# Kernel tuning notes

Hardware: AMD Instinct MI355X
Metric: run time of the kernel (lower is better)

The kernel has to match this reference:

```python
import jax, jax.numpy as jnp
import numpy as np

N_USERS = 100000
N_ITEMS = 50000
N_NODES = N_USERS + N_ITEMS
N_EDGES = 4800000
EMB = 64
N_LAYERS = 3
BATCH = 16384


def setup_inputs() -> dict:
    key = jax.random.key(0)
    ks = jax.random.split(key, 12)
    users = jax.random.randint(ks[0], (BATCH,), 0, N_USERS)
    pos_items = jax.random.randint(ks[1], (BATCH,), 0, N_ITEMS)
    neg_items = jax.random.randint(ks[2], (BATCH,), 0, N_ITEMS)
    rows = jax.random.randint(ks[3], (N_EDGES,), 0, N_NODES)
    cols = jax.random.randint(ks[4], (N_EDGES,), 0, N_NODES)
    vals = jax.random.uniform(ks[5], (N_EDGES,), dtype=jnp.float32)
    # learned parameters (xavier-ish scale)
    user_emb = jax.random.normal(ks[6], (N_USERS, EMB), dtype=jnp.float32) * 0.1
    item_emb = jax.random.normal(ks[7], (N_ITEMS, EMB), dtype=jnp.float32) * 0.1
    # Linear weights stored as [in, out] so y = x @ W + b (matches torch Linear math)
    W1s = jax.random.normal(ks[8], (N_LAYERS, EMB, EMB), dtype=jnp.float32) * (1.0 / np.sqrt(EMB))
    b1s = jnp.zeros((N_LAYERS, EMB), dtype=jnp.float32)
    W2s = jax.random.normal(ks[9], (N_LAYERS, EMB, EMB), dtype=jnp.float32) * (1.0 / np.sqrt(EMB))
    b2s = jnp.zeros((N_LAYERS, EMB), dtype=jnp.float32)
    return dict(users=users, pos_items=pos_items, neg_items=neg_items,
                rows=rows, cols=cols, vals=vals,
                user_emb=user_emb, item_emb=item_emb,
                W1s=W1s, b1s=b1s, W2s=W2s, b2s=b2s)


def _leaky_relu(x):
    return jnp.where(x > 0, x, 0.2 * x)


def _computer(user_emb, item_emb, rows, cols, vals, W1s, b1s, W2s, b2s):
    all_emb = jnp.concatenate([user_emb, item_emb], axis=0)  # [N, 64]
    embs = [all_emb]
    for i in range(N_LAYERS):
        self_emb = all_emb @ W1s[i] + b1s[i]
        # sparse adjacency SpMM: gather neighbor features, weight, segment-sum by row
        neighbor = jax.ops.segment_sum(vals[:, None] * all_emb[cols], rows,
                                       num_segments=N_NODES)
        neighbor = neighbor @ W2s[i] + b2s[i]
        interact = (neighbor * all_emb) @ W2s[i] + b2s[i]
        all_emb = _leaky_relu(self_emb + neighbor + interact)
        embs.append(all_emb)
    embs = jnp.concatenate(embs, axis=1)  # [N, 64*(n_layers+1)] = [N, 256]
    return embs[:N_USERS], embs[N_USERS:]


def reference(users, pos_items, neg_items, rows, cols, vals,
              user_emb, item_emb, W1s, b1s, W2s, b2s):
    all_users, all_items = _computer(user_emb, item_emb, rows, cols, vals,
                                     W1s, b1s, W2s, b2s)
    users_emb = all_users[users]
    pos_emb = all_items[pos_items]
    neg_emb = all_items[neg_items]
    return users_emb, pos_emb, neg_emb
```

## Files before the change

### kernel.cpp

```cpp
#include <hip/hip_runtime.h>


#define EMB 64

constexpr int kNUsers = 100000;
constexpr int kNItems = 50000;
constexpr int kNNodes = 150000;
constexpr int kNEdges = 4800000;
constexpr int kBatch  = 16384;
constexpr int kLayers = 3;
constexpr int kRngShift = 8;
constexpr int kNRanges  = (kNNodes + 255) >> 8;
constexpr int kEdgesPerBin = 16384;
constexpr int kBinBlocks = (kNEdges + kEdgesPerBin - 1) / kEdgesPerBin;
constexpr int kEPW    = 16;

__device__ __forceinline__ float f4c(const float4& v, int i) {
  return ((const float*)&v)[i];
}
__device__ __forceinline__ float4 f4fma(float s, float4 w, float4 a) {
  a.x = fmaf(s, w.x, a.x);
  a.y = fmaf(s, w.y, a.y);
  a.z = fmaf(s, w.z, a.z);
  a.w = fmaf(s, w.w, a.w);
  return a;
}
__device__ __forceinline__ float4 f4add(float4 a, float4 b) {
  a.x += b.x; a.y += b.y; a.z += b.z; a.w += b.w;
  return a;
}
__device__ __forceinline__ float lrelu(float x) { return x > 0.f ? x : 0.2f * x; }

#define F16(M) M(0) M(1) M(2) M(3) M(4) M(5) M(6) M(7) \
               M(8) M(9) M(10) M(11) M(12) M(13) M(14) M(15)

__global__ __launch_bounds__(256) void init_embed(
    const float* __restrict__ user_emb, const float* __restrict__ item_emb,
    float* __restrict__ cur)
{
  const size_t userF = (size_t)kNUsers * EMB;
  const size_t allF4 = (size_t)kNNodes * EMB / 4;
  const size_t i = (size_t)blockIdx.x * 256 + threadIdx.x;
  if (i >= allF4) return;
  const size_t f = i * 4;
  const float4 v = (f < userF) ? ((const float4*)user_emb)[i]
                               : ((const float4*)(item_emb))[(f - userF) / 4];
  ((float4*)cur)[i] = v;
}

__global__ __launch_bounds__(256) void quant8(
    const float* __restrict__ cur, signed char* __restrict__ cur8,
    float* __restrict__ rowScale)
{
  const int lane = threadIdx.x & 63;
  const int r = (blockIdx.x << 2) | (threadIdx.x >> 6);
  if (r >= kNNodes) return;
  const float v = cur[(size_t)r * EMB + lane];
  float m = fabsf(v);
#pragma unroll
  for (int off = 32; off >= 1; off >>= 1)
    m = fmaxf(m, __shfl_xor(m, off, 64));
  const float inv = (m > 0.f) ? (127.0f / m) : 0.f;
  cur8[(size_t)r * EMB + lane] = (signed char)__float2int_rn(v * inv);
  if (lane == 0) rowScale[r] = m * (1.0f / 127.0f);
}


__global__ __launch_bounds__(1024) void hist_ranges(
    const int* __restrict__ rows, int* __restrict__ rangeA)
{
  __shared__ int cnt[kNRanges];
  const int tid = threadIdx.x;
  const int e0  = blockIdx.x * kEdgesPerBin;
  int e1 = e0 + kEdgesPerBin;
  if (e1 > kNEdges) e1 = kNEdges;
  for (int b = tid; b < kNRanges; b += 1024) cnt[b] = 0;
  __syncthreads();
  for (int e = e0 + tid; e < e1; e += 1024)
    atomicAdd(&cnt[rows[e] >> kRngShift], 1);
  __syncthreads();
  for (int b = tid; b < kNRanges; b += 1024)
    if (cnt[b] > 0) atomicAdd(&rangeA[b], cnt[b]);
}

__global__ __launch_bounds__(1024) void scan_ranges(
    int* __restrict__ rangeA, int* __restrict__ rowPtr)
{
  __shared__ int wsum[16];
  const int tid  = threadIdx.x;
  const int lane = tid & 63;
  const int wid  = tid >> 6;
  const int cnt  = (tid < kNRanges) ? rangeA[tid] : 0;
  int v = cnt;
#pragma unroll
  for (int off = 1; off < 64; off <<= 1) {
    const int n = __shfl_up(v, off, 64);
    if (lane >= off) v += n;
  }
  if (lane == 63) wsum[wid] = v;
  __syncthreads();
  if (tid == 0) {
    int s = 0;
#pragma unroll
    for (int w = 0; w < 16; ++w) { const int t = wsum[w]; wsum[w] = s; s += t; }
  }
  __syncthreads();
  if (tid < kNRanges) rangeA[tid] = wsum[wid] + v - cnt;
  if (tid == 0) {
    rangeA[kNRanges]  = kNEdges;
    rowPtr[kNNodes]   = kNEdges;
  }
}

__global__ __launch_bounds__(1024) void bin_edges(
    const int* __restrict__ rows, const int* __restrict__ cols,
    const float* __restrict__ vals, const int* __restrict__ rangeA,
    int* __restrict__ rangeCnt, int2* __restrict__ tmpE)
{
  __shared__ int cnt[kNRanges];
  __shared__ int base[kNRanges];
  const int tid = threadIdx.x;
  const int e0  = blockIdx.x * kEdgesPerBin;
  int e1 = e0 + kEdgesPerBin;
  if (e1 > kNEdges) e1 = kNEdges;

  for (int b = tid; b < kNRanges; b += 1024) cnt[b] = 0;
  __syncthreads();
  for (int e = e0 + tid; e < e1; e += 1024)
    atomicAdd(&cnt[rows[e] >> kRngShift], 1);
  __syncthreads();
  for (int b = tid; b < kNRanges; b += 1024) {
    const int c = cnt[b];
    base[b] = (c > 0) ? (rangeA[b] + atomicAdd(&rangeCnt[b], c)) : 0;
    cnt[b] = 0;
  }
  __syncthreads();
  for (int e = e0 + tid; e < e1; e += 1024) {
    const int r = rows[e];
    const int b = r >> kRngShift;
    const int rank = atomicAdd(&cnt[b], 1);
    tmpE[base[b] + rank] =
        make_int2(cols[e] | ((r & 255) << 18), __float_as_int(vals[e]));
  }
}

__global__ __launch_bounds__(256) void place_edges(
    const int2* __restrict__ tmpE, const int* __restrict__ rangeA,
    int2* __restrict__ edgeS, int* __restrict__ rowPtr)
{
  __shared__ int lcnt[256];
  __shared__ int lbase[256];
  __shared__ int ws[4];
  const int b    = blockIdx.x;
  const int r0   = b << kRngShift;
  const int tid  = threadIdx.x;
  const int lane = tid & 63;
  const int wid  = tid >> 6;
  const int start = rangeA[b];
  const int end   = rangeA[b + 1];

  lcnt[tid] = 0;
  __syncthreads();
  for (int e = start + tid; e < end; e += 256)
    atomicAdd(&lcnt[(tmpE[e].x >> 18) & 255], 1);
  __syncthreads();

  const int c = lcnt[tid];
  int v = c;
#pragma unroll
  for (int off = 1; off < 64; off <<= 1) {
    const int n = __shfl_up(v, off, 64);
    if (lane >= off) v += n;
  }
  if (lane == 63) ws[wid] = v;
  __syncthreads();
  int wadd = 0;
#pragma unroll
  for (int w = 0; w < 4; ++w) if (w < wid) wadd += ws[w];
  const int excl = v - c + wadd;
  lbase[tid] = start + excl;
  if (r0 + tid < kNNodes) rowPtr[r0 + tid] = start + excl;
  lcnt[tid] = 0;
  __syncthreads();

  for (int e = start + tid; e < end; e += 256) {
    const int2 cv = tmpE[e];
    const int rl  = (cv.x >> 18) & 255;
    const int rank = atomicAdd(&lcnt[rl], 1);
    edgeS[lbase[rl] + rank] = make_int2(cv.x & 0x3FFFF, cv.y);
  }
}

__global__ __launch_bounds__(256) void spmm_csr8(
    const signed char* __restrict__ cur8, const float* __restrict__ rowScale,
    const int* __restrict__ rowPtr, const int2* __restrict__ edgeS,
    float* __restrict__ nbuf)
{
  const int lane = threadIdx.x & 63;
  const int r = (blockIdx.x << 2) | (threadIdx.x >> 6);
  if (r >= kNNodes) return;
  const int start = __builtin_amdgcn_readfirstlane(rowPtr[r]);
  const int end   = __builtin_amdgcn_readfirstlane(rowPtr[r + 1]);
  float a0 = 0.f, a1 = 0.f, a2 = 0.f, a3 = 0.f;
  int e = start;
  for (; e + 4 <= end; e += 4) {
    const int2 cv0 = edgeS[e];
    const int2 cv1 = edgeS[e + 1];
    const int2 cv2 = edgeS[e + 2];
    const int2 cv3 = edgeS[e + 3];
    const int q0 = cur8[(size_t)cv0.x * EMB + lane];
    const int q1 = cur8[(size_t)cv1.x * EMB + lane];
    const int q2 = cur8[(size_t)cv2.x * EMB + lane];
    const int q3 = cur8[(size_t)cv3.x * EMB + lane];
    const float s0 = __int_as_float(cv0.y) * rowScale[cv0.x];
    const float s1 = __int_as_float(cv1.y) * rowScale[cv1.x];
    const float s2 = __int_as_float(cv2.y) * rowScale[cv2.x];
    const float s3 = __int_as_float(cv3.y) * rowScale[cv3.x];
    a0 = fmaf(s0, (float)q0, a0);
    a1 = fmaf(s1, (float)q1, a1);
    a2 = fmaf(s2, (float)q2, a2);
    a3 = fmaf(s3, (float)q3, a3);
  }
  for (; e < end; ++e) {
    const int2 cv = edgeS[e];
    const int q = cur8[(size_t)cv.x * EMB + lane];
    a0 = fmaf(__int_as_float(cv.y) * rowScale[cv.x], (float)q, a0);
  }
  nbuf[(size_t)r * EMB + lane] = (a0 + a1) + (a2 + a3);
}

__global__ __launch_bounds__(256) void spmm_csr(
    const float* __restrict__ cur, const int* __restrict__ rowPtr,
    const int2* __restrict__ edgeS, float* __restrict__ nbuf)
{
  const int lane = threadIdx.x & 63;
  const int r = (blockIdx.x << 2) | (threadIdx.x >> 6);
  if (r >= kNNodes) return;
  const int start = __builtin_amdgcn_readfirstlane(rowPtr[r]);
  const int end   = __builtin_amdgcn_readfirstlane(rowPtr[r + 1]);
  float a0 = 0.f, a1 = 0.f, a2 = 0.f, a3 = 0.f;
  int e = start;
  for (; e + 4 <= end; e += 4) {
    const int2 cv0 = edgeS[e];
    const int2 cv1 = edgeS[e + 1];
    const int2 cv2 = edgeS[e + 2];
    const int2 cv3 = edgeS[e + 3];
    a0 = fmaf(__int_as_float(cv0.y), cur[(size_t)cv0.x * EMB + lane], a0);
    a1 = fmaf(__int_as_float(cv1.y), cur[(size_t)cv1.x * EMB + lane], a1);
    a2 = fmaf(__int_as_float(cv2.y), cur[(size_t)cv2.x * EMB + lane], a2);
    a3 = fmaf(__int_as_float(cv3.y), cur[(size_t)cv3.x * EMB + lane], a3);
  }
  for (; e < end; ++e) {
    const int2 cv = edgeS[e];
    a0 = fmaf(__int_as_float(cv.y), cur[(size_t)cv.x * EMB + lane], a0);
  }
  nbuf[(size_t)r * EMB + lane] = (a0 + a1) + (a2 + a3);
}

__global__ __launch_bounds__(256) void spmm_atomic(
    const float* __restrict__ cur, const int* __restrict__ rows,
    const int* __restrict__ cols, const float* __restrict__ vals,
    float* __restrict__ nbuf)
{
  const int lane = threadIdx.x & 63;
  int wv = (blockIdx.x << 2) | (threadIdx.x >> 6);
  wv = __builtin_amdgcn_readfirstlane(wv);
  int e0 = wv * kEPW;
  int e1 = e0 + kEPW;
  if (e1 > kNEdges) e1 = kNEdges;
  for (int e = e0; e < e1; ++e) {
    atomicAdd(nbuf + (size_t)rows[e] * EMB + lane,
              vals[e] * cur[(size_t)cols[e] * EMB + lane]);
  }
}

__global__ __launch_bounds__(256) void transform_nbr(
    float* __restrict__ nbuf, const float* __restrict__ W2,
    const float* __restrict__ b2)
{
  const int node = blockIdx.x * 256 + threadIdx.x;
  if (node >= kNNodes) return;
  const float4* __restrict__ nr  = (const float4*)(nbuf + (size_t)node * EMB);
  const float4* __restrict__ b2v = (const float4*)b2;
#define DECL(j) float4 a##j = b2v[j];
  F16(DECL)
#undef DECL
#pragma unroll 4
  for (int k4 = 0; k4 < 16; ++k4) {
    const float4 nv = nr[k4];
#pragma unroll
    for (int kk = 0; kk < 4; ++kk) {
      const float ns = f4c(nv, kk);
      const float4* __restrict__ w2r = (const float4*)(W2 + (4 * k4 + kk) * EMB);
#define STEP(j) a##j = f4fma(ns, w2r[j], a##j);
      F16(STEP)
#undef STEP
    }
  }
  float4* __restrict__ outp = (float4*)(nbuf + (size_t)node * EMB);
#define STORE(j) outp[j] = a##j;
  F16(STORE)
#undef STORE
}

__global__ __launch_bounds__(256) void transform_self(
    float* __restrict__ cur, const float* __restrict__ nbuf,
    const float* __restrict__ W1, const float* __restrict__ b1,
    const float* __restrict__ b2, const float* __restrict__ W2)
{
  const int node = blockIdx.x * 256 + threadIdx.x;
  if (node >= kNNodes) return;
  const float4* __restrict__ xr  = (const float4*)(cur  + (size_t)node * EMB);
  const float4* __restrict__ tr  = (const float4*)(nbuf + (size_t)node * EMB);
  const float4* __restrict__ b1v = (const float4*)b1;
  const float4* __restrict__ b2v = (const float4*)b2;
#define DECL(j) float4 a##j = f4add(b1v[j], b2v[j]);
  F16(DECL)
#undef DECL
#pragma unroll 2
  for (int k4 = 0; k4 < 16; ++k4) {
    const float4 xv = xr[k4];
    const float4 tv = tr[k4];
#pragma unroll
    for (int kk = 0; kk < 4; ++kk) {
      const float xs = f4c(xv, kk);
      const float ms = f4c(tv, kk) * xs;
      const int k = 4 * k4 + kk;
      const float4* __restrict__ w1r = (const float4*)(W1 + k * EMB);
      const float4* __restrict__ w2r = (const float4*)(W2 + k * EMB);
#define STEP(j) a##j = f4fma(xs, w1r[j], a##j); a##j = f4fma(ms, w2r[j], a##j);
      F16(STEP)
#undef STEP
    }
  }
  float4* __restrict__ outp = (float4*)(cur + (size_t)node * EMB);
#define STORE(j) { const float4 tj = tr[j]; float4 r;          \
    r.x = lrelu(a##j.x + tj.x); r.y = lrelu(a##j.y + tj.y);    \
    r.z = lrelu(a##j.z + tj.z); r.w = lrelu(a##j.w + tj.w);    \
    outp[j] = r; }
  F16(STORE)
#undef STORE
}

__global__ __launch_bounds__(256) void gather_out(
    const float* __restrict__ cur, const int* __restrict__ users,
    const int* __restrict__ pos, const int* __restrict__ neg,
    float* __restrict__ out, int layer)
{
  const int t    = blockIdx.x * 256 + threadIdx.x;
  const int lane = t & 63;
  const int rid  = t >> 6;
  if (rid >= 3 * kBatch) return;
  const int seg = rid / kBatch;
  const int b   = rid - seg * kBatch;
  int idx;
  if (seg == 0)      idx = users[b];
  else if (seg == 1) idx = pos[b] + kNUsers;
  else               idx = neg[b] + kNUsers;
  out[(size_t)rid * 256 + layer * EMB + lane] = cur[(size_t)idx * EMB + lane];
}

extern "C" void kernel_launch(void* const* d_in, const int* in_sizes, int n_in,
                              void* d_out, int out_size, void* d_ws, size_t ws_size,
                              hipStream_t stream) {
  const int*   users    = (const int*)d_in[0];
  const int*   pos      = (const int*)d_in[1];
  const int*   neg      = (const int*)d_in[2];
  const int*   rows     = (const int*)d_in[3];
  const int*   cols     = (const int*)d_in[4];
  const float* vals     = (const float*)d_in[5];
  const float* user_emb = (const float*)d_in[6];
  const float* item_emb = (const float*)d_in[7];
  const float* W1s      = (const float*)d_in[8];
  const float* b1s      = (const float*)d_in[9];
  const float* W2s      = (const float*)d_in[10];
  const float* b2s      = (const float*)d_in[11];
  float* out = (float*)d_out;

  const size_t nodeF = (size_t)kNNodes * EMB;
  float* cur  = (float*)d_ws;
  float* nbuf = cur + nodeF;
  int2*  edgeS     = (int2*)(nbuf + nodeF);
  int*   rowPtr    = (int*)(edgeS + kNEdges);
  int*   rangeA    = rowPtr + (kNNodes + 1);
  int*   rangeCnt  = rangeA + (kNRanges + 1);
  signed char* cur8 = (signed char*)(rangeCnt + kNRanges);
  float* rowScale  = (float*)(cur8 + nodeF);
  int2*  tmpE = (int2*)nbuf;
  const size_t neededCsr = (size_t)((char*)cur8 - (char*)d_ws);
  const size_t needed8   = (size_t)((char*)(rowScale + kNNodes) - (char*)d_ws);
  const bool useCsr = ws_size >= neededCsr;
  const bool use8   = useCsr && ws_size >= needed8;

  const dim3 blk(256);
  const int iblocks = (int)((nodeF / 4 + 255) / 256);
  const int gblocks = (3 * kBatch * EMB + 255) / 256;
  const int rblocks = (kNNodes + 3) / 4;
  const int tblocks = (kNNodes + 255) / 256;

  init_embed<<<iblocks, blk, 0, stream>>>(user_emb, item_emb, cur);
  if (use8)
    quant8<<<rblocks, blk, 0, stream>>>(cur, cur8, rowScale);

  if (useCsr) {
    hipMemsetAsync(rangeA, 0, (size_t)(2 * kNRanges + 1) * sizeof(int), stream);
    hist_ranges<<<kBinBlocks, dim3(1024), 0, stream>>>(rows, rangeA);
    scan_ranges<<<1, 1024, 0, stream>>>(rangeA, rowPtr);
    bin_edges<<<kBinBlocks, dim3(1024), 0, stream>>>(rows, cols, vals, rangeA,
                                                     rangeCnt, tmpE);
    place_edges<<<kNRanges, blk, 0, stream>>>(tmpE, rangeA, edgeS, rowPtr);
  }

  gather_out<<<gblocks, blk, 0, stream>>>(cur, users, pos, neg, out, 0);

  for (int L = 0; L < kLayers; ++L) {
    if (useCsr) {
      if (use8)
        spmm_csr8<<<rblocks, blk, 0, stream>>>(cur8, rowScale, rowPtr, edgeS,
                                               nbuf);
      else
        spmm_csr<<<rblocks, blk, 0, stream>>>(cur, rowPtr, edgeS, nbuf);
    } else {
      hipMemsetAsync(nbuf, 0, nodeF * sizeof(float), stream);
      const int sblocks = (((kNEdges + kEPW - 1) / kEPW) + 3) / 4;
      spmm_atomic<<<sblocks, blk, 0, stream>>>(cur, rows, cols, vals, nbuf);
    }
    transform_nbr<<<tblocks, blk, 0, stream>>>(
        nbuf, W2s + L * EMB * EMB, b2s + L * EMB);
    transform_self<<<tblocks, blk, 0, stream>>>(
        cur, nbuf, W1s + L * EMB * EMB, b1s + L * EMB,
        b2s + L * EMB, W2s + L * EMB * EMB);
    if (use8 && L + 1 < kLayers)
      quant8<<<rblocks, blk, 0, stream>>>(cur, cur8, rowScale);
    gather_out<<<gblocks, blk, 0, stream>>>(cur, users, pos, neg, out, L + 1);
  }
}
```

Before: 1.340 ms.

## Split CSR SpMM into three column-range passes for gather cache locality

Edges within each row are partitioned into three column slices, and per-row slice boundaries are stored in an extra pointer array. The SpMM then runs as three passes, each touching only one third of the int8 embedding table, so the gather working set may fit better in L2/LLC. The cost is reading and writing the output buffer three times and launching three kernels instead of one. The fp32 CSR fallback is removed, so only the int8 path remains.

```diff
diff --git a/kernel.cpp b/kernel.cpp
--- a/kernel.cpp
+++ b/kernel.cpp
@@ -13,6 +13,8 @@
 constexpr int kNRanges  = (kNNodes + 255) >> 8;
 constexpr int kEdgesPerBin = 16384;
 constexpr int kBinBlocks = (kNEdges + kEdgesPerBin - 1) / kEdgesPerBin;
+constexpr int kSlice1 = 50000;
+constexpr int kSlice2 = 100000;
 constexpr int kEPW    = 16;
 
 __device__ __forceinline__ float f4c(const float4& v, int i) {
@@ -146,10 +148,10 @@
 
 __global__ __launch_bounds__(256) void place_edges(
     const int2* __restrict__ tmpE, const int* __restrict__ rangeA,
-    int2* __restrict__ edgeS, int* __restrict__ rowPtr)
-{
-  __shared__ int lcnt[256];
-  __shared__ int lbase[256];
+    int2* __restrict__ edgeS, int* __restrict__ rowPtr,
+    int* __restrict__ rowPtrS)
+{
+  __shared__ int lcnt[256][4];
   __shared__ int ws[4];
   const int b    = blockIdx.x;
   const int r0   = b << kRngShift;
@@ -159,13 +161,20 @@
   const int start = rangeA[b];
   const int end   = rangeA[b + 1];
 
-  lcnt[tid] = 0;
-  __syncthreads();
-  for (int e = start + tid; e < end; e += 256)
-    atomicAdd(&lcnt[(tmpE[e].x >> 18) & 255], 1);
-  __syncthreads();
-
-  const int c = lcnt[tid];
+  lcnt[tid][0] = 0; lcnt[tid][1] = 0; lcnt[tid][2] = 0;
+  __syncthreads();
+  for (int e = start + tid; e < end; e += 256) {
+    const int cv  = tmpE[e].x;
+    const int col = cv & 0x3FFFF;
+    const int s   = (col >= kSlice2) ? 2 : ((col >= kSlice1) ? 1 : 0);
+    atomicAdd(&lcnt[(cv >> 18) & 255][s], 1);
+  }
+  __syncthreads();
+
+  const int c0 = lcnt[tid][0];
+  const int c1 = lcnt[tid][1];
+  const int c2 = lcnt[tid][2];
+  const int c  = c0 + c1 + c2;
   int v = c;
 #pragma unroll
   for (int off = 1; off < 64; off <<= 1) {
@@ -177,30 +186,38 @@
   int wadd = 0;
 #pragma unroll
   for (int w = 0; w < 4; ++w) if (w < wid) wadd += ws[w];
-  const int excl = v - c + wadd;
-  lbase[tid] = start + excl;
-  if (r0 + tid < kNNodes) rowPtr[r0 + tid] = start + excl;
-  lcnt[tid] = 0;
+  const int rbase = start + v - c + wadd;
+  if (r0 + tid < kNNodes) {
+    rowPtr[r0 + tid] = rbase;
+    rowPtrS[r0 + tid]           = rbase + c0;
+    rowPtrS[kNNodes + r0 + tid] = rbase + c0 + c1;
+  }
+  __syncthreads();
+  lcnt[tid][0] = rbase;
+  lcnt[tid][1] = rbase + c0;
+  lcnt[tid][2] = rbase + c0 + c1;
   __syncthreads();
 
   for (int e = start + tid; e < end; e += 256) {
     const int2 cv = tmpE[e];
     const int rl  = (cv.x >> 18) & 255;
-    const int rank = atomicAdd(&lcnt[rl], 1);
-    edgeS[lbase[rl] + rank] = make_int2(cv.x & 0x3FFFF, cv.y);
-  }
-}
-
-__global__ __launch_bounds__(256) void spmm_csr8(
+    const int col = cv.x & 0x3FFFF;
+    const int s   = (col >= kSlice2) ? 2 : ((col >= kSlice1) ? 1 : 0);
+    const int slot = atomicAdd(&lcnt[rl][s], 1);
+    edgeS[slot] = make_int2(col, cv.y);
+  }
+}
+
+__global__ __launch_bounds__(256) void spmm_pass8(
     const signed char* __restrict__ cur8, const float* __restrict__ rowScale,
-    const int* __restrict__ rowPtr, const int2* __restrict__ edgeS,
-    float* __restrict__ nbuf)
+    const int* __restrict__ startPtr, const int* __restrict__ endPtr,
+    const int2* __restrict__ edgeS, float* __restrict__ nbuf, int accFlag)
 {
   const int lane = threadIdx.x & 63;
   const int r = (blockIdx.x << 2) | (threadIdx.x >> 6);
   if (r >= kNNodes) return;
-  const int start = __builtin_amdgcn_readfirstlane(rowPtr[r]);
-  const int end   = __builtin_amdgcn_readfirstlane(rowPtr[r + 1]);
+  const int start = __builtin_amdgcn_readfirstlane(startPtr[r]);
+  const int end   = __builtin_amdgcn_readfirstlane(endPtr[r]);
   float a0 = 0.f, a1 = 0.f, a2 = 0.f, a3 = 0.f;
   int e = start;
   for (; e + 4 <= end; e += 4) {
@@ -226,35 +243,10 @@
     const int q = cur8[(size_t)cv.x * EMB + lane];
     a0 = fmaf(__int_as_float(cv.y) * rowScale[cv.x], (float)q, a0);
   }
-  nbuf[(size_t)r * EMB + lane] = (a0 + a1) + (a2 + a3);
-}
-
-__global__ __launch_bounds__(256) void spmm_csr(
-    const float* __restrict__ cur, const int* __restrict__ rowPtr,
-    const int2* __restrict__ edgeS, float* __restrict__ nbuf)
-{
-  const int lane = threadIdx.x & 63;
-  const int r = (blockIdx.x << 2) | (threadIdx.x >> 6);
-  if (r >= kNNodes) return;
-  const int start = __builtin_amdgcn_readfirstlane(rowPtr[r]);
-  const int end   = __builtin_amdgcn_readfirstlane(rowPtr[r + 1]);
-  float a0 = 0.f, a1 = 0.f, a2 = 0.f, a3 = 0.f;
-  int e = start;
-  for (; e + 4 <= end; e += 4) {
-    const int2 cv0 = edgeS[e];
-    const int2 cv1 = edgeS[e + 1];
-    const int2 cv2 = edgeS[e + 2];
-    const int2 cv3 = edgeS[e + 3];
-    a0 = fmaf(__int_as_float(cv0.y), cur[(size_t)cv0.x * EMB + lane], a0);
-    a1 = fmaf(__int_as_float(cv1.y), cur[(size_t)cv1.x * EMB + lane], a1);
-    a2 = fmaf(__int_as_float(cv2.y), cur[(size_t)cv2.x * EMB + lane], a2);
-    a3 = fmaf(__int_as_float(cv3.y), cur[(size_t)cv3.x * EMB + lane], a3);
-  }
-  for (; e < end; ++e) {
-    const int2 cv = edgeS[e];
-    a0 = fmaf(__int_as_float(cv.y), cur[(size_t)cv.x * EMB + lane], a0);
-  }
-  nbuf[(size_t)r * EMB + lane] = (a0 + a1) + (a2 + a3);
+  float sum = (a0 + a1) + (a2 + a3);
+  float* p = nbuf + (size_t)r * EMB + lane;
+  if (accFlag) sum += *p;
+  *p = sum;
 }
 
 __global__ __launch_bounds__(256) void spmm_atomic(
@@ -384,13 +376,12 @@
   int*   rowPtr    = (int*)(edgeS + kNEdges);
   int*   rangeA    = rowPtr + (kNNodes + 1);
   int*   rangeCnt  = rangeA + (kNRanges + 1);
-  signed char* cur8 = (signed char*)(rangeCnt + kNRanges);
+  int*   rowPtrS   = rangeCnt + kNRanges;
+  signed char* cur8 = (signed char*)(rowPtrS + 2 * kNNodes);
   float* rowScale  = (float*)(cur8 + nodeF);
   int2*  tmpE = (int2*)nbuf;
-  const size_t neededCsr = (size_t)((char*)cur8 - (char*)d_ws);
-  const size_t needed8   = (size_t)((char*)(rowScale + kNNodes) - (char*)d_ws);
-  const bool useCsr = ws_size >= neededCsr;
-  const bool use8   = useCsr && ws_size >= needed8;
+  const size_t needed = (size_t)((char*)(rowScale + kNNodes) - (char*)d_ws);
+  const bool useCsr = ws_size >= needed;
 
   const dim3 blk(256);
   const int iblocks = (int)((nodeF / 4 + 255) / 256);
@@ -399,27 +390,28 @@
   const int tblocks = (kNNodes + 255) / 256;
 
   init_embed<<<iblocks, blk, 0, stream>>>(user_emb, item_emb, cur);
-  if (use8)
+
+  if (useCsr) {
     quant8<<<rblocks, blk, 0, stream>>>(cur, cur8, rowScale);
-
-  if (useCsr) {
     hipMemsetAsync(rangeA, 0, (size_t)(2 * kNRanges + 1) * sizeof(int), stream);
     hist_ranges<<<kBinBlocks, dim3(1024), 0, stream>>>(rows, rangeA);
     scan_ranges<<<1, 1024, 0, stream>>>(rangeA, rowPtr);
     bin_edges<<<kBinBlocks, dim3(1024), 0, stream>>>(rows, cols, vals, rangeA,
                                                      rangeCnt, tmpE);
-    place_edges<<<kNRanges, blk, 0, stream>>>(tmpE, rangeA, edgeS, rowPtr);
+    place_edges<<<kNRanges, blk, 0, stream>>>(tmpE, rangeA, edgeS, rowPtr,
+                                              rowPtrS);
   }
 
   gather_out<<<gblocks, blk, 0, stream>>>(cur, users, pos, neg, out, 0);
 
   for (int L = 0; L < kLayers; ++L) {
     if (useCsr) {
-      if (use8)
-        spmm_csr8<<<rblocks, blk, 0, stream>>>(cur8, rowScale, rowPtr, edgeS,
-                                               nbuf);
-      else
-        spmm_csr<<<rblocks, blk, 0, stream>>>(cur, rowPtr, edgeS, nbuf);
+      spmm_pass8<<<rblocks, blk, 0, stream>>>(cur8, rowScale, rowPtr, rowPtrS,
+                                              edgeS, nbuf, 0);
+      spmm_pass8<<<rblocks, blk, 0, stream>>>(cur8, rowScale, rowPtrS,
+                                              rowPtrS + kNNodes, edgeS, nbuf, 1);
+      spmm_pass8<<<rblocks, blk, 0, stream>>>(cur8, rowScale, rowPtrS + kNNodes,
+                                              rowPtr + 1, edgeS, nbuf, 1);
     } else {
       hipMemsetAsync(nbuf, 0, nodeF * sizeof(float), stream);
       const int sblocks = (((kNEdges + kEPW - 1) / kEPW) + 3) / 4;
@@ -430,7 +422,7 @@
     transform_self<<<tblocks, blk, 0, stream>>>(
         cur, nbuf, W1s + L * EMB * EMB, b1s + L * EMB,
         b2s + L * EMB, W2s + L * EMB * EMB);
-    if (use8 && L + 1 < kLayers)
+    if (useCsr && L + 1 < kLayers)
       quant8<<<rblocks, blk, 0, stream>>>(cur, cur8, rowScale);
     gather_out<<<gblocks, blk, 0, stream>>>(cur, users, pos, neg, out, L + 1);
   }
```

Result: slower. 1.477 ms (+10.2%).
